# Optimization experiments

Hardware: AMD Instinct MI355X
Metric: run time of the kernel (lower is better)

## Reference

```python
import jax, jax.numpy as jnp
import numpy as np

N = 65536
EMB_DIM = 1024
PICK_NUM = 12  # ceil(ln(65536)) = ceil(11.09) = 12


def setup_inputs() -> dict:
    key = jax.random.key(0)
    k_emb, k_wq, k_bq, k_wk, k_bk, k_idx = jax.random.split(key, 6)
    s = 1.0 / np.sqrt(EMB_DIM)
    embed_matrix = jax.random.normal(k_emb, (N, EMB_DIM), dtype=jnp.float32)
    Wq = jax.random.normal(k_wq, (EMB_DIM, EMB_DIM), dtype=jnp.float32) * s
    bq = jax.random.normal(k_bq, (EMB_DIM,), dtype=jnp.float32) * s
    Wk = jax.random.normal(k_wk, (EMB_DIM, EMB_DIM), dtype=jnp.float32) * s
    bk = jax.random.normal(k_bk, (EMB_DIM,), dtype=jnp.float32) * s
    # np.random.choice(n, pick_num, replace=False) -> deterministic permutation slice
    indices = jax.random.permutation(k_idx, N)[:PICK_NUM].astype(jnp.int32)
    return {"embed_matrix": embed_matrix, "Wq": Wq, "bq": bq,
            "Wk": Wk, "bk": bk, "indices": indices}


def reference(embed_matrix, Wq, bq, Wk, bk, indices):
    pick_num = indices.shape[0]
    # torch.nn.Linear: y = x @ W.T + b
    query = embed_matrix @ Wq.T + bq          # [n, d]
    key = embed_matrix @ Wk.T + bk            # [n, d]
    new_key = key[indices]                    # [pick, d] sampled keys
    Q_K_sample = query @ new_key.T            # [n, pick]
    max_values = jnp.max(Q_K_sample, axis=1)  # [n]
    _, top_indices = jax.lax.top_k(max_values, pick_num)
    Q_reduced = query[top_indices]            # [pick, d]
    Q_K = Q_reduced @ key.T                   # [pick, n]
    pooled = jnp.max(Q_K, axis=0, keepdims=True)  # [1, n]
    attention_embed = pooled @ embed_matrix   # [1, d]
    return attention_embed
```

## Files before the change

kernel.cpp:

```cpp
#include <hip/hip_runtime.h>

#define DIM 1024
#define NROWS 65536
#define PICK 12


__global__ void __launch_bounds__(256)
rows12_kernel(const float* __restrict__ emb, const float* __restrict__ W,
              const float* __restrict__ b, const int* __restrict__ idx,
              float* __restrict__ out) {
    int d = blockIdx.x;
    int t = threadIdx.x;
    int lane = t & 63;
    int q = t >> 6;
    int e0 = q * 256 + lane * 4;
    float4 w4 = *(const float4*)&W[(size_t)d * DIM + e0];
    float part[PICK];
#pragma unroll
    for (int j = 0; j < PICK; ++j) {
        int r = idx[j];
        float4 e4 = *(const float4*)&emb[(size_t)r * DIM + e0];
        part[j] = w4.x * e4.x + w4.y * e4.y + w4.z * e4.z + w4.w * e4.w;
    }
#pragma unroll
    for (int j = 0; j < PICK; ++j) {
        float v = part[j];
        for (int s = 32; s > 0; s >>= 1) v += __shfl_down(v, s, 64);
        part[j] = v;
    }
    __shared__ float red[4][PICK];
    if (lane == 0) {
#pragma unroll
        for (int j = 0; j < PICK; ++j) red[q][j] = part[j];
    }
    __syncthreads();
    if (t < PICK) {
        float s = red[0][t] + red[1][t] + red[2][t] + red[3][t] + b[d];
        out[t * DIM + d] = s;
    }
}

__global__ void __launch_bounds__(256)
colmat_kernel(const float* __restrict__ W, const float* __restrict__ V,
              const float* __restrict__ b, float* __restrict__ out,
              float* __restrict__ cvec) {
    int blk = blockIdx.x;
    int t = threadIdx.x;
    if (blk == 128) {
        float part[PICK];
#pragma unroll
        for (int j = 0; j < PICK; ++j) part[j] = 0.f;
        for (int k = 0; k < 4; ++k) {
            int d = t + k * 256;
            float bv = b[d];
#pragma unroll
            for (int j = 0; j < PICK; ++j) part[j] += bv * V[j * DIM + d];
        }
#pragma unroll
        for (int j = 0; j < PICK; ++j) {
            float v = part[j];
            for (int s = 32; s > 0; s >>= 1) v += __shfl_down(v, s, 64);
            if ((t & 63) == 0) atomicAdd(&cvec[j], v);
        }
        return;
    }
    int eg = blk & 3;
    int dg = blk >> 2;
    int e = eg * 256 + t;
    int d0 = dg * 32;
    __shared__ float Vs[PICK][32];
    for (int i = t; i < PICK * 32; i += 256) {
        int j = i >> 5, dd = i & 31;
        Vs[j][dd] = V[j * DIM + d0 + dd];
    }
    __syncthreads();
    float acc[PICK];
#pragma unroll
    for (int j = 0; j < PICK; ++j) acc[j] = 0.f;
    for (int dd = 0; dd < 32; ++dd) {
        float w = W[(size_t)(d0 + dd) * DIM + e];
#pragma unroll
        for (int j = 0; j < PICK; ++j) acc[j] += w * Vs[j][dd];
    }
#pragma unroll
    for (int j = 0; j < PICK; ++j) atomicAdd(&out[j * DIM + e], acc[j]);
}


#define PG(BUF, G, PAR, SINK)                                                 \
  {                                                                           \
    float acc[2][PICK];                                                       \
    _Pragma("unroll") for (int r = 0; r < 2; ++r)                             \
      _Pragma("unroll") for (int j = 0; j < PICK; ++j) acc[r][j] = 0.f;       \
    _Pragma("unroll") for (int c = 0; c < 4; ++c) {                           \
      float4 m4[PICK];                                                        \
      _Pragma("unroll") for (int j = 0; j < PICK; ++j)                        \
        m4[j] = *(const float4*)&sMt[j * DIM + c * 256 + l * 4];              \
      _Pragma("unroll") for (int r = 0; r < 2; ++r) {                         \
        float4 vv = BUF[r][c];                                                \
        _Pragma("unroll") for (int j = 0; j < PICK; ++j)                      \
          acc[r][j] += vv.x * m4[j].x + vv.y * m4[j].y + vv.z * m4[j].z +     \
                       vv.w * m4[j].w;                                        \
      }                                                                       \
    }                                                                         \
    _Pragma("unroll") for (int r = 0; r < 2; ++r)                             \
      _Pragma("unroll") for (int j = 0; j < PICK; ++j) {                      \
        float v1 = acc[r][j];                                                 \
        v1 += __shfl_xor(v1, 1, 64);                                          \
        v1 += __shfl_xor(v1, 2, 64);                                          \
        acc[r][j] = v1;                                                       \
      }                                                                       \
    if ((l & 3) == 0) {                                                       \
      _Pragma("unroll") for (int jh = 0; jh < 6; ++jh) {                      \
        float4 b4 = {acc[0][2 * jh], acc[1][2 * jh], acc[0][2 * jh + 1],      \
                     acc[1][2 * jh + 1]};                                     \
        *(float4*)&scr[PAR][w][q][jh * 4] = b4;                               \
      }                                                                       \
    }                                                                         \
    asm volatile("s_waitcnt lgkmcnt(0)" ::: "memory");                        \
    float sum = 0.f;                                                          \
    _Pragma("unroll") for (int qq = 0; qq < 16; ++qq)                         \
      sum += scr[PAR][w][qq][pidx];                                           \
    float vmax = (p < 24) ? sum + cb : -3e38f;                                \
    _Pragma("unroll") for (int mm = 2; mm <= 16; mm <<= 1)                    \
      vmax = fmaxf(vmax, __shfl_xor(vmax, mm, 64));                           \
    if (p < 2) SINK = vmax;                                                   \
  }

__global__ void __launch_bounds__(256, 2)
pass1_kernel(const float* __restrict__ emb, const float* __restrict__ Mt,
             const float* __restrict__ c0, float* __restrict__ maxv) {
    __shared__ __align__(16) float sMt[PICK * DIM];
    __shared__ __align__(16) float scr[2][4][16][28];
    int t = threadIdx.x;
    for (int i = t; i < PICK * DIM / 4; i += 256)
        ((float4*)sMt)[i] = ((const float4*)Mt)[i];
    __syncthreads();

    int l = t & 63, w = t >> 6;
    int q = l >> 2;
    int p = l;
    int pidx = (p < 24) ? p : 0;
    float cb = (p < 24) ? c0[p >> 1] : 0.f;
    size_t wrow = (size_t)blockIdx.x * 128 + (size_t)w * 32;
    const float* base = emb + wrow * DIM + l * 4;

    float4 A[2][4], B[2][4];
#pragma unroll
    for (int r = 0; r < 2; ++r)
#pragma unroll
      for (int c = 0; c < 4; ++c)
        A[r][c] = *(const float4*)(base + (size_t)r * DIM + c * 256);

    for (int gg = 0; gg < 8; ++gg) {
#pragma unroll
        for (int r = 0; r < 2; ++r)
#pragma unroll
          for (int c = 0; c < 4; ++c)
            B[r][c] = *(const float4*)(base + ((size_t)(2 * gg + 1) * 2 + r) * DIM + c * 256);
        PG(A, 2 * gg, 0, maxv[wrow + (2 * gg) * 2 + p]);
        if (gg < 7) {
#pragma unroll
            for (int r = 0; r < 2; ++r)
#pragma unroll
              for (int c = 0; c < 4; ++c)
                A[r][c] = *(const float4*)(base + ((size_t)(2 * gg + 2) * 2 + r) * DIM + c * 256);
        }
        PG(B, 2 * gg + 1, 1, maxv[wrow + (2 * gg + 1) * 2 + p]);
    }
}

__global__ void __launch_bounds__(256, 2)
pass2_kernel(const float* __restrict__ emb, const float* __restrict__ Rt,
             const float* __restrict__ c1, float* __restrict__ out) {
    __shared__ __align__(16) float sMt[PICK * DIM];
    __shared__ __align__(16) float scr[2][4][16][28];
    __shared__ float pooled[128];
    int t = threadIdx.x;
    for (int i = t; i < PICK * DIM / 4; i += 256)
        ((float4*)sMt)[i] = ((const float4*)Rt)[i];
    __syncthreads();

    int l = t & 63, w = t >> 6;
    int q = l >> 2;
    int p = l;
    int pidx = (p < 24) ? p : 0;
    float cb = (p < 24) ? c1[p >> 1] : 0.f;
    size_t bbase = (size_t)blockIdx.x * 128;
    size_t wrow = bbase + (size_t)w * 32;
    const float* base = emb + wrow * DIM + l * 4;

    float4 A[2][4], B[2][4];
#pragma unroll
    for (int r = 0; r < 2; ++r)
#pragma unroll
      for (int c = 0; c < 4; ++c)
        A[r][c] = *(const float4*)(base + (size_t)r * DIM + c * 256);

    for (int gg = 0; gg < 8; ++gg) {
#pragma unroll
        for (int r = 0; r < 2; ++r)
#pragma unroll
          for (int c = 0; c < 4; ++c)
            B[r][c] = *(const float4*)(base + ((size_t)(2 * gg + 1) * 2 + r) * DIM + c * 256);
        PG(A, 2 * gg, 0, pooled[w * 32 + (2 * gg) * 2 + p]);
        if (gg < 7) {
#pragma unroll
            for (int r = 0; r < 2; ++r)
#pragma unroll
              for (int c = 0; c < 4; ++c)
                A[r][c] = *(const float4*)(base + ((size_t)(2 * gg + 2) * 2 + r) * DIM + c * 256);
        }
        PG(B, 2 * gg + 1, 1, pooled[w * 32 + (2 * gg + 1) * 2 + p]);
    }
    __syncthreads();

    const float* tp = emb + bbase * DIM + t * 4;
    float4 o = {0.f, 0.f, 0.f, 0.f};
#pragma unroll 8
    for (int r = 0; r < 128; ++r) {
        float pv = pooled[r];
        float4 v = *(const float4*)(tp + (size_t)r * DIM);
        o.x += pv * v.x; o.y += pv * v.y; o.z += pv * v.z; o.w += pv * v.w;
    }
    atomicAdd(&out[t * 4 + 0], o.x);
    atomicAdd(&out[t * 4 + 1], o.y);
    atomicAdd(&out[t * 4 + 2], o.z);
    atomicAdd(&out[t * 4 + 3], o.w);
}

__global__ void __launch_bounds__(64)
top12_local(const float* __restrict__ maxv, float* __restrict__ cand_v,
            int* __restrict__ cand_i) {
    int t = threadIdx.x;
    int base = blockIdx.x * 1024;
    float lv[16];
#pragma unroll
    for (int q = 0; q < 16; ++q) lv[q] = maxv[base + q * 64 + t];
    for (int k = 0; k < PICK; ++k) {
        float bv = -3e38f; int bi = 0x7fffffff;
#pragma unroll
        for (int q = 0; q < 16; ++q) {
            int ii = base + q * 64 + t;
            float v = lv[q];
            if (v > bv || (v == bv && ii < bi)) { bv = v; bi = ii; }
        }
#pragma unroll
        for (int sft = 1; sft < 64; sft <<= 1) {
            float ov = __shfl_xor(bv, sft, 64);
            int oi = __shfl_xor(bi, sft, 64);
            if (ov > bv || (ov == bv && oi < bi)) { bv = ov; bi = oi; }
        }
        if (t == 0) {
            cand_v[blockIdx.x * PICK + k] = bv;
            cand_i[blockIdx.x * PICK + k] = bi;
        }
#pragma unroll
        for (int q = 0; q < 16; ++q)
            if (base + q * 64 + t == bi) lv[q] = -3e38f;
    }
}

__global__ void __launch_bounds__(64)
top12_merge(const float* __restrict__ cand_v, const int* __restrict__ cand_i,
            int* __restrict__ top_idx) {
    int t = threadIdx.x;
    float lv[12]; int li[12];
#pragma unroll
    for (int q = 0; q < 12; ++q) {
        lv[q] = cand_v[q * 64 + t];
        li[q] = cand_i[q * 64 + t];
    }
    for (int k = 0; k < PICK; ++k) {
        float bv = -3e38f; int bi = 0x7fffffff; int bs = -1;
#pragma unroll
        for (int q = 0; q < 12; ++q) {
            if (lv[q] > bv || (lv[q] == bv && li[q] < bi)) {
                bv = lv[q]; bi = li[q]; bs = q * 64 + t;
            }
        }
#pragma unroll
        for (int sft = 1; sft < 64; sft <<= 1) {
            float ov = __shfl_xor(bv, sft, 64);
            int oi = __shfl_xor(bi, sft, 64);
            int os = __shfl_xor(bs, sft, 64);
            if (ov > bv || (ov == bv && oi < bi)) { bv = ov; bi = oi; bs = os; }
        }
        if (t == 0) top_idx[k] = bi;
#pragma unroll
        for (int q = 0; q < 12; ++q)
            if (q * 64 + t == bs) lv[q] = -3e38f;
    }
}

extern "C" void kernel_launch(void* const* d_in, const int* in_sizes, int n_in,
                              void* d_out, int out_size, void* d_ws, size_t ws_size,
                              hipStream_t stream) {
    const float* emb = (const float*)d_in[0];
    const float* Wq  = (const float*)d_in[1];
    const float* bq  = (const float*)d_in[2];
    const float* Wk  = (const float*)d_in[3];
    const float* bk  = (const float*)d_in[4];
    const int* indices = (const int*)d_in[5];
    float* out = (float*)d_out;
    float* ws = (float*)d_ws;

    float* NK      = ws;
    float* Qr      = ws + 12288;
    float* Mt      = ws + 24576;
    float* Rt      = ws + 36864;
    float* c0      = ws + 49152;
    float* c1      = ws + 49168;
    float* cand_v  = ws + 49184;
    int*   cand_i  = (int*)(ws + 49952);
    int*   top_idx = (int*)(ws + 50720);
    float* maxv    = ws + 50736;

    hipMemsetAsync(Mt, 0, (size_t)(12288 * 2 + 32) * sizeof(float), stream);
    hipMemsetAsync(out, 0, DIM * sizeof(float), stream);

    rows12_kernel<<<1024, 256, 0, stream>>>(emb, Wk, bk, indices, NK);
    colmat_kernel<<<129, 256, 0, stream>>>(Wq, NK, bq, Mt, c0);
    pass1_kernel<<<512, 256, 0, stream>>>(emb, Mt, c0, maxv);
    top12_local<<<64, 64, 0, stream>>>(maxv, cand_v, cand_i);
    top12_merge<<<1, 64, 0, stream>>>(cand_v, cand_i, top_idx);
    rows12_kernel<<<1024, 256, 0, stream>>>(emb, Wq, bq, top_idx, Qr);
    colmat_kernel<<<129, 256, 0, stream>>>(Wk, Qr, bk, Rt, c1);
    pass2_kernel<<<512, 256, 0, stream>>>(emb, Rt, c1, out);
}
```

Before: 555.1 us.

## Restructure row loop into 8-row tiles to reuse LDS weight loads

The pass1 and pass2 inner loops now handle 8 rows per tile instead of 2 rows per group. Each load of the 12 projected key vectors from LDS is reused across 8 rows, which cuts LDS read traffic per FLOP by about 4x. A double-buffered column-chunk prefetch of the next rows replaces the old two-buffer row prefetch. The cost is a 96-float accumulator per thread, which raises register pressure and could lower occupancy under launch_bounds(256,2) or cause spills.

```diff
diff --git a/kernel.cpp b/kernel.cpp
--- a/kernel.cpp
+++ b/kernel.cpp
@@ -87,33 +87,34 @@
 }
 
 
-#define PG(BUF, G, PAR, SINK)                                                 \
+#define CHUNK(CBUF, NBUF, CC, PF_ROW, PF_CHUNK)                               \
   {                                                                           \
-    float acc[2][PICK];                                                       \
-    _Pragma("unroll") for (int r = 0; r < 2; ++r)                             \
-      _Pragma("unroll") for (int j = 0; j < PICK; ++j) acc[r][j] = 0.f;       \
-    _Pragma("unroll") for (int c = 0; c < 4; ++c) {                           \
-      float4 m4[PICK];                                                        \
-      _Pragma("unroll") for (int j = 0; j < PICK; ++j)                        \
-        m4[j] = *(const float4*)&sMt[j * DIM + c * 256 + l * 4];              \
-      _Pragma("unroll") for (int r = 0; r < 2; ++r) {                         \
-        float4 vv = BUF[r][c];                                                \
-        _Pragma("unroll") for (int j = 0; j < PICK; ++j)                      \
-          acc[r][j] += vv.x * m4[j].x + vv.y * m4[j].y + vv.z * m4[j].z +     \
-                       vv.w * m4[j].w;                                        \
-      }                                                                       \
+    _Pragma("unroll") for (int r = 0; r < 8; ++r)                             \
+      NBUF[r] = *(const float4*)(emb + (size_t)((PF_ROW) + r) * DIM +         \
+                                 (PF_CHUNK) * 256 + l * 4);                   \
+    float4 m4[12];                                                            \
+    _Pragma("unroll") for (int j = 0; j < 12; ++j)                            \
+      m4[j] = *(const float4*)&sMt[j * DIM + (CC) * 256 + l * 4];             \
+    _Pragma("unroll") for (int r = 0; r < 8; ++r) {                           \
+      float f0 = CBUF[r].x, f1 = CBUF[r].y, f2 = CBUF[r].z, f3 = CBUF[r].w;   \
+      _Pragma("unroll") for (int j = 0; j < 12; ++j)                          \
+        acc[r][j] += f0 * m4[j].x + f1 * m4[j].y + f2 * m4[j].z +             \
+                     f3 * m4[j].w;                                            \
     }                                                                         \
-    _Pragma("unroll") for (int r = 0; r < 2; ++r)                             \
-      _Pragma("unroll") for (int j = 0; j < PICK; ++j) {                      \
-        float v1 = acc[r][j];                                                 \
-        v1 += __shfl_xor(v1, 1, 64);                                          \
-        v1 += __shfl_xor(v1, 2, 64);                                          \
-        acc[r][j] = v1;                                                       \
-      }                                                                       \
+  }
+
+#define EPI(R0, PAR, SINK)                                                    \
+  {                                                                           \
+    float a0[PICK], a1[PICK];                                                 \
+    _Pragma("unroll") for (int j = 0; j < PICK; ++j) {                        \
+      float v0 = acc[R0][j], v1 = acc[R0 + 1][j];                             \
+      v0 += __shfl_xor(v0, 1, 64); v0 += __shfl_xor(v0, 2, 64);               \
+      v1 += __shfl_xor(v1, 1, 64); v1 += __shfl_xor(v1, 2, 64);               \
+      a0[j] = v0; a1[j] = v1;                                                 \
+    }                                                                         \
     if ((l & 3) == 0) {                                                       \
       _Pragma("unroll") for (int jh = 0; jh < 6; ++jh) {                      \
-        float4 b4 = {acc[0][2 * jh], acc[1][2 * jh], acc[0][2 * jh + 1],      \
-                     acc[1][2 * jh + 1]};                                     \
+        float4 b4 = {a0[2 * jh], a1[2 * jh], a0[2 * jh + 1], a1[2 * jh + 1]}; \
         *(float4*)&scr[PAR][w][q][jh * 4] = b4;                               \
       }                                                                       \
     }                                                                         \
@@ -143,30 +144,30 @@
     int pidx = (p < 24) ? p : 0;
     float cb = (p < 24) ? c0[p >> 1] : 0.f;
     size_t wrow = (size_t)blockIdx.x * 128 + (size_t)w * 32;
-    const float* base = emb + wrow * DIM + l * 4;
-
-    float4 A[2][4], B[2][4];
-#pragma unroll
-    for (int r = 0; r < 2; ++r)
-#pragma unroll
-      for (int c = 0; c < 4; ++c)
-        A[r][c] = *(const float4*)(base + (size_t)r * DIM + c * 256);
-
-    for (int gg = 0; gg < 8; ++gg) {
-#pragma unroll
-        for (int r = 0; r < 2; ++r)
-#pragma unroll
-          for (int c = 0; c < 4; ++c)
-            B[r][c] = *(const float4*)(base + ((size_t)(2 * gg + 1) * 2 + r) * DIM + c * 256);
-        PG(A, 2 * gg, 0, maxv[wrow + (2 * gg) * 2 + p]);
-        if (gg < 7) {
-#pragma unroll
-            for (int r = 0; r < 2; ++r)
-#pragma unroll
-              for (int c = 0; c < 4; ++c)
-                A[r][c] = *(const float4*)(base + ((size_t)(2 * gg + 2) * 2 + r) * DIM + c * 256);
-        }
-        PG(B, 2 * gg + 1, 1, maxv[wrow + (2 * gg + 1) * 2 + p]);
+
+    float4 bufA[8], bufB[8];
+#pragma unroll
+    for (int r = 0; r < 8; ++r)
+        bufA[r] = *(const float4*)(emb + (wrow + r) * DIM + l * 4);
+
+    for (int tile = 0; tile < 4; ++tile) {
+        size_t trow = wrow + (size_t)tile * 8;
+        size_t ntrow = wrow + (size_t)((tile < 3) ? tile + 1 : 3) * 8;
+        float acc[8][PICK];
+#pragma unroll
+        for (int r = 0; r < 8; ++r)
+#pragma unroll
+            for (int j = 0; j < PICK; ++j) acc[r][j] = 0.f;
+
+        CHUNK(bufA, bufB, 0, trow, 1);
+        CHUNK(bufB, bufA, 1, trow, 2);
+        CHUNK(bufA, bufB, 2, trow, 3);
+        CHUNK(bufB, bufA, 3, ntrow, 0);
+
+        EPI(0, 0, maxv[trow + 0 + p]);
+        EPI(2, 1, maxv[trow + 2 + p]);
+        EPI(4, 0, maxv[trow + 4 + p]);
+        EPI(6, 1, maxv[trow + 6 + p]);
     }
 }
 
@@ -188,30 +189,30 @@
     float cb = (p < 24) ? c1[p >> 1] : 0.f;
     size_t bbase = (size_t)blockIdx.x * 128;
     size_t wrow = bbase + (size_t)w * 32;
-    const float* base = emb + wrow * DIM + l * 4;
-
-    float4 A[2][4], B[2][4];
-#pragma unroll
-    for (int r = 0; r < 2; ++r)
-#pragma unroll
-      for (int c = 0; c < 4; ++c)
-        A[r][c] = *(const float4*)(base + (size_t)r * DIM + c * 256);
-
-    for (int gg = 0; gg < 8; ++gg) {
-#pragma unroll
-        for (int r = 0; r < 2; ++r)
-#pragma unroll
-          for (int c = 0; c < 4; ++c)
-            B[r][c] = *(const float4*)(base + ((size_t)(2 * gg + 1) * 2 + r) * DIM + c * 256);
-        PG(A, 2 * gg, 0, pooled[w * 32 + (2 * gg) * 2 + p]);
-        if (gg < 7) {
-#pragma unroll
-            for (int r = 0; r < 2; ++r)
-#pragma unroll
-              for (int c = 0; c < 4; ++c)
-                A[r][c] = *(const float4*)(base + ((size_t)(2 * gg + 2) * 2 + r) * DIM + c * 256);
-        }
-        PG(B, 2 * gg + 1, 1, pooled[w * 32 + (2 * gg + 1) * 2 + p]);
+
+    float4 bufA[8], bufB[8];
+#pragma unroll
+    for (int r = 0; r < 8; ++r)
+        bufA[r] = *(const float4*)(emb + (wrow + r) * DIM + l * 4);
+
+    for (int tile = 0; tile < 4; ++tile) {
+        size_t trow = wrow + (size_t)tile * 8;
+        size_t ntrow = wrow + (size_t)((tile < 3) ? tile + 1 : 3) * 8;
+        float acc[8][PICK];
+#pragma unroll
+        for (int r = 0; r < 8; ++r)
+#pragma unroll
+            for (int j = 0; j < PICK; ++j) acc[r][j] = 0.f;
+
+        CHUNK(bufA, bufB, 0, trow, 1);
+        CHUNK(bufB, bufA, 1, trow, 2);
+        CHUNK(bufA, bufB, 2, trow, 3);
+        CHUNK(bufB, bufA, 3, ntrow, 0);
+
+        EPI(0, 0, pooled[w * 32 + tile * 8 + 0 + p]);
+        EPI(2, 1, pooled[w * 32 + tile * 8 + 2 + p]);
+        EPI(4, 0, pooled[w * 32 + tile * 8 + 4 + p]);
+        EPI(6, 1, pooled[w * 32 + tile * 8 + 6 + p]);
     }
     __syncthreads();
 
```

Result: slower. 1.888 ms (+240.1%).
